# Performance work log

Hardware: AMD Instinct MI355X
Metric: run time of the kernel (lower is better)

The kernel has to match this reference:

```python
import jax, jax.numpy as jnp
import numpy as np

DIM, N_HEADS, N_EXPERTS, TOP_K = 1024, 16, 8, 2
D_FF = 4 * DIM
HEAD_DIM = DIM // N_HEADS
EPS = 1e-5


def layer_norm(x, g, b):
    m = x.mean(-1, keepdims=True)
    v = ((x - m) ** 2).mean(-1, keepdims=True)
    return (x - m) / jnp.sqrt(v + EPS) * g + b


def setup_inputs() -> dict:
    key = jax.random.key(0)
    ks = jax.random.split(key, 16)
    B, T = 8, 1024
    s = 0.02
    inp = {
        'x': jax.random.normal(ks[0], (B, T, DIM), jnp.float32),
        'attention_mask': jnp.ones((B, T), jnp.int32),
        'Wq': jax.random.normal(ks[1], (DIM, DIM), jnp.float32) * s,
        'bq': jnp.zeros((DIM,), jnp.float32),
        'Wk': jax.random.normal(ks[2], (DIM, DIM), jnp.float32) * s,
        'bk': jnp.zeros((DIM,), jnp.float32),
        'Wv': jax.random.normal(ks[3], (DIM, DIM), jnp.float32) * s,
        'bv': jnp.zeros((DIM,), jnp.float32),
        'Wo': jax.random.normal(ks[4], (DIM, DIM), jnp.float32) * s,
        'bo': jnp.zeros((DIM,), jnp.float32),
        'g1': jnp.ones((DIM,), jnp.float32),
        'beta1': jnp.zeros((DIM,), jnp.float32),
        'router_w': jax.random.normal(ks[5], (DIM, N_EXPERTS), jnp.float32) * s,
        'router_b': jnp.zeros((N_EXPERTS,), jnp.float32),
        'W1': jax.random.normal(ks[6], (N_EXPERTS, DIM, D_FF), jnp.float32) * s,
        'B1': jnp.zeros((N_EXPERTS, D_FF), jnp.float32),
        'W2': jax.random.normal(ks[7], (N_EXPERTS, D_FF, DIM), jnp.float32) * s,
        'B2': jnp.zeros((N_EXPERTS, DIM), jnp.float32),
        'g2': jnp.ones((DIM,), jnp.float32),
        'beta2': jnp.zeros((DIM,), jnp.float32),
    }
    return inp


def reference(x, attention_mask, Wq, bq, Wk, bk, Wv, bv, Wo, bo, g1, beta1,
              router_w, router_b, W1, B1, W2, B2, g2, beta2):
    B, T, D = x.shape
    H, hd = N_HEADS, HEAD_DIM
    # ---- multi-head attention with causal + padding mask ----
    q = (x @ Wq + bq).reshape(B, T, H, hd).transpose(0, 2, 1, 3)  # [B,H,T,hd]
    k = (x @ Wk + bk).reshape(B, T, H, hd).transpose(0, 2, 1, 3)
    v = (x @ Wv + bv).reshape(B, T, H, hd).transpose(0, 2, 1, 3)
    scores = jnp.einsum('bhqd,bhkd->bhqk', q, k) / jnp.sqrt(jnp.float32(hd))
    causal = jnp.tril(jnp.ones((T, T), bool))[None, None]            # [1,1,T,T]
    mask = causal & (attention_mask[:, None, None, :] != 0)         # [B,1,T,T]
    scores = jnp.where(mask, scores, jnp.float32(-1e9))
    attn = jax.nn.softmax(scores, axis=-1)
    h = jnp.einsum('bhqk,bhkd->bhqd', attn, v).transpose(0, 2, 1, 3).reshape(B, T, D)
    h = h @ Wo + bo
    # dropout is identity in eval mode
    x1 = layer_norm(x + h, g1, beta1)
    # ---- sparse top-k MoE FFN ----
    xf = x1.reshape(-1, D)                                           # [N,D]
    logits = xf @ router_w + router_b                                # [N,E]
    probs = jax.nn.softmax(logits, axis=-1)
    topv, topi = jax.lax.top_k(probs, TOP_K)                         # [N,k]
    gk = topv / topv.sum(-1, keepdims=True)                          # renormalized gates
    onehot = jax.nn.one_hot(topi, N_EXPERTS, dtype=xf.dtype)         # [N,k,E]
    gates = (onehot * gk[..., None]).sum(1)                          # [N,E]
    y = jnp.zeros_like(xf)
    for e in range(N_EXPERTS):  # fixed small expert loop
        he = jax.nn.relu(xf @ W1[e] + B1[e])
        y = y + gates[:, e:e + 1] * (he @ W2[e] + B2[e])
    # load-balancing loss: E * sum_i f_i * P_i
    f = onehot.sum(1).mean(0)                                        # fraction routed per expert
    P = probs.mean(0)
    lb = jnp.float32(N_EXPERTS) * (f * P).sum()
    out = layer_norm(x1 + y.reshape(B, T, D), g2, beta2)
    return out, lb
```

## Files before the change

### kernel.cpp

```cpp
#include <hip/hip_runtime.h>
#include <hip/hip_bf16.h>
#include <stdint.h>

#define DIMQ   1024
#define NHEADS 16
#define HD     64
#define NEXP   8
#define DFF    4096
#define NTOK   8192
#define TSEQ   1024
#define BATCH  8

typedef unsigned short u16;
typedef unsigned int   u32;
typedef __attribute__((ext_vector_type(8))) short bf16x8;
typedef __attribute__((ext_vector_type(4))) float f32x4;

__device__ __forceinline__ float bf_lo(u32 w) { return __uint_as_float(w << 16); }
__device__ __forceinline__ float bf_hi(u32 w) { return __uint_as_float(w & 0xffff0000u); }
__device__ __forceinline__ u16 f2bf(float f) {
  u32 x = __float_as_uint(f);
  return (u16)((x + 0x7fffu + ((x >> 16) & 1u)) >> 16);
}

__device__ __forceinline__ void gload16(const u16* g, u16* l) {
  __builtin_amdgcn_global_load_lds((const __attribute__((address_space(1))) u32*)g,
                                   (__attribute__((address_space(3))) u32*)l, 16, 0, 0);
}

__global__ __launch_bounds__(256) void cvt_f32_bf16(const float* __restrict__ in,
                                                    u16* __restrict__ out, int n) {
  int i = (blockIdx.x * 256 + threadIdx.x) * 4;
  if (i >= n) return;
  float4 v = *(const float4*)(in + i);
  ushort4 o;
  o.x = f2bf(v.x); o.y = f2bf(v.y); o.z = f2bf(v.z); o.w = f2bf(v.w);
  *(ushort4*)(out + i) = o;
}

__global__ __launch_bounds__(256) void transpose_f32_bf16(
    const float* __restrict__ in, u16* __restrict__ out, int R, int C) {
  __shared__ float tile[32][33];
  size_t base = (size_t)blockIdx.z * (size_t)R * (size_t)C;
  int tx = threadIdx.x & 31, ty = threadIdx.x >> 5;
  int c = blockIdx.x * 32 + tx;
#pragma unroll
  for (int i = 0; i < 4; i++) {
    int r = blockIdx.y * 32 + ty + i * 8;
    tile[ty + i * 8][tx] = in[base + (size_t)r * C + c];
  }
  __syncthreads();
  int rr = blockIdx.y * 32 + tx;
#pragma unroll
  for (int i = 0; i < 4; i++) {
    int cc = blockIdx.x * 32 + ty + i * 8;
    out[base + (size_t)cc * R + rr] = f2bf(tile[tx][ty + i * 8]);
  }
}

template <bool GATHER, bool RELU, bool TRANSC>
__device__ __forceinline__ void gemm_core(
    const u16* __restrict__ A, const u16* __restrict__ Bt,
    const float* __restrict__ bias, u16* __restrict__ C,
    int M, int N, int K, const int* __restrict__ gidx) {
  __shared__ u16 As[2][128 * 32];
  __shared__ u16 Bs[2][128 * 32];
  const int tid = threadIdx.x;
  const int lane = tid & 63;
  const int wave = tid >> 6;
  const int wr = wave >> 1, wc = wave & 1;
  const int lr = lane & 15, kg = lane >> 4;
  const int rowbase = blockIdx.y * 128;
  const int colbase = blockIdx.x * 128;

  f32x4 acc[4][4];
#pragma unroll
  for (int m = 0; m < 4; m++)
#pragma unroll
    for (int n = 0; n < 4; n++) acc[m][n] = (f32x4){0.f, 0.f, 0.f, 0.f};

  const int r0 = tid >> 2, seg = tid & 3;
  const int slog = seg ^ ((r0 >> 1) & 3);
  int ar0 = rowbase + r0;      if (ar0 >= M) ar0 = M - 1;
  int ar1 = rowbase + r0 + 64; if (ar1 >= M) ar1 = M - 1;
  const long arow0 = GATHER ? gidx[ar0] : ar0;
  const long arow1 = GATHER ? gidx[ar1] : ar1;
  const u16* Aptr0 = A + (size_t)arow0 * K + slog * 8;
  const u16* Aptr1 = A + (size_t)arow1 * K + slog * 8;
  const u16* Bptr0 = Bt + (size_t)(colbase + r0) * K + slog * 8;
  const u16* Bptr1 = Bt + (size_t)(colbase + r0 + 64) * K + slog * 8;

  const int swz = (lr >> 1) & 3;

#define STAGE128(buf, k0)                                   \
  {                                                         \
    gload16(Aptr0 + (k0), &As[buf][tid * 8]);               \
    gload16(Aptr1 + (k0), &As[buf][2048 + tid * 8]);        \
    gload16(Bptr0 + (k0), &Bs[buf][tid * 8]);               \
    gload16(Bptr1 + (k0), &Bs[buf][2048 + tid * 8]);        \
  }

  const int NT = K >> 5;
  STAGE128(0, 0);
  STAGE128(1, 32);
  for (int t = 0; t < NT; t++) {
    const int buf = t & 1;
    if (t + 1 < NT) asm volatile("s_waitcnt vmcnt(4)" ::: "memory");
    else            asm volatile("s_waitcnt vmcnt(0)" ::: "memory");
    __builtin_amdgcn_s_barrier();
    bf16x8 af[4], bfr[4];
#pragma unroll
    for (int m = 0; m < 4; m++)
      af[m] = *(const bf16x8*)(&As[buf][(wr * 64 + m * 16 + lr) * 32 + ((kg ^ swz) * 8)]);
#pragma unroll
    for (int n = 0; n < 4; n++)
      bfr[n] = *(const bf16x8*)(&Bs[buf][(wc * 64 + n * 16 + lr) * 32 + ((kg ^ swz) * 8)]);
#pragma unroll
    for (int m = 0; m < 4; m++)
#pragma unroll
      for (int n = 0; n < 4; n++)
        acc[m][n] = __builtin_amdgcn_mfma_f32_16x16x32_bf16(af[m], bfr[n], acc[m][n], 0, 0, 0);
    __builtin_amdgcn_s_barrier();
    if (t + 2 < NT) STAGE128(buf, (t + 2) << 5);
  }
#undef STAGE128

#pragma unroll
  for (int n = 0; n < 4; n++) {
    int col = colbase + wc * 64 + n * 16 + lr;
    float bv = bias[col];
#pragma unroll
    for (int m = 0; m < 4; m++) {
      int row0 = rowbase + wr * 64 + m * 16 + kg * 4;
      if (TRANSC) {
        if (row0 + 3 < M) {
          ushort4 pk;
          pk.x = f2bf(acc[m][n][0] + bv);
          pk.y = f2bf(acc[m][n][1] + bv);
          pk.z = f2bf(acc[m][n][2] + bv);
          pk.w = f2bf(acc[m][n][3] + bv);
          *(ushort4*)(&C[(size_t)col * M + row0]) = pk;
        } else {
#pragma unroll
          for (int r = 0; r < 4; r++)
            if (row0 + r < M) C[(size_t)col * M + row0 + r] = f2bf(acc[m][n][r] + bv);
        }
      } else {
#pragma unroll
        for (int r = 0; r < 4; r++) {
          int row = row0 + r;
          if (row < M) {
            float v = acc[m][n][r] + bv;
            if (RELU) v = fmaxf(v, 0.f);
            C[(size_t)row * N + col] = f2bf(v);
          }
        }
      }
    }
  }
}

__global__ __launch_bounds__(256) void gemm_bt_kernel(
    const u16* __restrict__ A, const u16* __restrict__ Bt,
    const float* __restrict__ bias, u16* __restrict__ C, int M, int N, int K) {
  gemm_core<false, false, false>(A, Bt, bias, C, M, N, K, nullptr);
}

__global__ __launch_bounds__(256) void gemm_bt_tc_kernel(
    const u16* __restrict__ A, const u16* __restrict__ Bt,
    const float* __restrict__ bias, u16* __restrict__ C, int M, int N, int K) {
  gemm_core<false, false, true>(A, Bt, bias, C, M, N, K, nullptr);
}

template <bool GATHER, bool RELU>
__device__ __forceinline__ void gemm256_core(
    const u16* __restrict__ A, const u16* __restrict__ Bt,
    const float* __restrict__ bias, u16* __restrict__ C,
    int M, int N, int K, const int* __restrict__ gidx) {
  __shared__ u16 lds[2][2][256 * 64];
  const int tid = threadIdx.x;
  const int lane = tid & 63;
  const int wave = tid >> 6;
  const int wr = wave >> 2;
  const int wcol = wave & 3;
  const int lr = lane & 15, kg = lane >> 4;
  const int rowbase = blockIdx.y * 256;
  const int colbase = blockIdx.x * 256;

  f32x4 acc[8][4];
#pragma unroll
  for (int m = 0; m < 8; m++)
#pragma unroll
    for (int n = 0; n < 4; n++) acc[m][n] = (f32x4){0.f, 0.f, 0.f, 0.f};

  const int srow0 = tid >> 3, sphys = tid & 7;
  const u16* asrc[4];
  const u16* bsrc[4];
#pragma unroll
  for (int j = 0; j < 4; j++) {
    int row = srow0 + j * 64;
    int ls = sphys ^ (row & 7);
    int ar = rowbase + row; if (ar >= M) ar = M - 1;
    long ga = GATHER ? gidx[ar] : ar;
    asrc[j] = A + (size_t)ga * K + ls * 8;
    bsrc[j] = Bt + (size_t)(colbase + row) * K + ls * 8;
  }

#define STAGE256(buf, k0)                                              \
  {                                                                    \
    _Pragma("unroll")                                                  \
    for (int j = 0; j < 4; j++) {                                      \
      gload16(asrc[j] + (k0), &lds[buf][0][tid * 8 + j * 4096]);       \
      gload16(bsrc[j] + (k0), &lds[buf][1][tid * 8 + j * 4096]);       \
    }                                                                  \
  }

  const int NT = K >> 6;
  STAGE256(0, 0);
  STAGE256(1, 64);
  for (int t = 0; t < NT; t++) {
    const int buf = t & 1;
    if (t + 1 < NT) asm volatile("s_waitcnt vmcnt(8)" ::: "memory");
    else            asm volatile("s_waitcnt vmcnt(0)" ::: "memory");
    __builtin_amdgcn_s_barrier();
    bf16x8 bfr[4][2];
#pragma unroll
    for (int nr = 0; nr < 4; nr++) {
      int rb = wcol * 64 + nr * 16 + lr;
#pragma unroll
      for (int kk = 0; kk < 2; kk++)
        bfr[nr][kk] = *(const bf16x8*)(&lds[buf][1][rb * 64 + (((kk * 4 + kg) ^ (rb & 7)) * 8)]);
    }
    __builtin_amdgcn_s_setprio(1);
#pragma unroll
    for (int mr = 0; mr < 8; mr++) {
      int ra = wr * 128 + mr * 16 + lr;
      bf16x8 a0 = *(const bf16x8*)(&lds[buf][0][ra * 64 + ((kg ^ (ra & 7)) * 8)]);
      bf16x8 a1 = *(const bf16x8*)(&lds[buf][0][ra * 64 + (((4 + kg) ^ (ra & 7)) * 8)]);
#pragma unroll
      for (int nr = 0; nr < 4; nr++) {
        acc[mr][nr] = __builtin_amdgcn_mfma_f32_16x16x32_bf16(a0, bfr[nr][0], acc[mr][nr], 0, 0, 0);
        acc[mr][nr] = __builtin_amdgcn_mfma_f32_16x16x32_bf16(a1, bfr[nr][1], acc[mr][nr], 0, 0, 0);
      }
    }
    __builtin_amdgcn_s_setprio(0);
    __builtin_amdgcn_s_barrier();
    if (t + 2 < NT) STAGE256(buf, (t + 2) << 6);
  }
#undef STAGE256

#pragma unroll
  for (int nr = 0; nr < 4; nr++) {
    int col = colbase + wcol * 64 + nr * 16 + lr;
    float bv = bias[col];
#pragma unroll
    for (int mr = 0; mr < 8; mr++) {
      int row0 = rowbase + wr * 128 + mr * 16 + kg * 4;
#pragma unroll
      for (int r = 0; r < 4; r++) {
        int row = row0 + r;
        if (row < M) {
          float v = acc[mr][nr][r] + bv;
          if (RELU) v = fmaxf(v, 0.f);
          C[(size_t)row * N + col] = f2bf(v);
        }
      }
    }
  }
}

__global__ __launch_bounds__(512, 2) void moe_gemm1_kernel(
    const u16* __restrict__ x1b, const u16* __restrict__ W1t,
    const float* __restrict__ B1, u16* __restrict__ he,
    const int* __restrict__ cnt, const int* __restrict__ off,
    const int* __restrict__ idxlist) {
  int e = blockIdx.z;
  int M = cnt[e];
  if ((int)blockIdx.y * 256 >= M) return;
  gemm256_core<true, true>(x1b, W1t + (size_t)e * DFF * DIMQ, B1 + e * DFF,
                           he + (size_t)off[e] * DFF, M, DFF, DIMQ, idxlist + off[e]);
}

__global__ __launch_bounds__(512, 2) void moe_gemm2_kernel(
    const u16* __restrict__ he, const u16* __restrict__ W2t,
    const float* __restrict__ B2, u16* __restrict__ yslot,
    const int* __restrict__ cnt, const int* __restrict__ off) {
  int e = blockIdx.z;
  int M = cnt[e];
  if ((int)blockIdx.y * 256 >= M) return;
  gemm256_core<false, false>(he + (size_t)off[e] * DFF, W2t + (size_t)e * DIMQ * DFF,
                             B2 + e * DIMQ, yslot + (size_t)off[e] * DIMQ, M, DIMQ, DFF, nullptr);
}

__global__ __launch_bounds__(256) void attn_mfma_kernel(
    const u16* __restrict__ qb, const u16* __restrict__ kb,
    const u16* __restrict__ vbT, const int* __restrict__ amask,
    u16* __restrict__ hb) {
  __shared__ u16 Ks[32 * 64];
  __shared__ u16 VTs[64 * 32];
  __shared__ u16 Ps[4][16 * 32];
  __shared__ float mbias[32];

  const int b = blockIdx.y >> 4;
  const int h = blockIdx.y & 15;
  const int qb0 = blockIdx.x * 64;
  const int tid = threadIdx.x;
  const int lane = tid & 63;
  const int wq = tid >> 6;
  const int r16 = lane & 15;
  const int kg = lane >> 4;
  const int qrow0 = qb0 + wq * 16;

  bf16x8 qf[2];
  {
    const u16* qp = qb + ((size_t)(b * TSEQ + qrow0 + r16)) * DIMQ + h * HD + kg * 8;
    qf[0] = *(const bf16x8*)(qp);
    qf[1] = *(const bf16x8*)(qp + 32);
  }
  f32x4 acc[4];
#pragma unroll
  for (int db = 0; db < 4; db++) acc[db] = (f32x4){0.f, 0.f, 0.f, 0.f};
  float m_run[4], l_run[4];
#pragma unroll
  for (int i = 0; i < 4; i++) { m_run[i] = -3.0e38f; l_run[i] = 0.f; }

  const int skey = tid >> 3, sslot = tid & 7;
  const int sd = tid >> 2, sko = tid & 3;
  const u16* kgb = kb + (size_t)(b * TSEQ) * DIMQ + h * HD;
  const u16* vgb = vbT + (size_t)(h * HD) * NTOK + (size_t)b * TSEQ;

  const int nt = (qb0 + 64) >> 5;
  for (int kt = 0; kt < nt; kt++) {
    const int k0g = kt * 32;
    __syncthreads();
    {
      uint4 kv = *(const uint4*)(kgb + (size_t)(k0g + skey) * DIMQ + sslot * 8);
      *(uint4*)(&Ks[skey * 64 + ((sslot ^ (skey & 7)) * 8)]) = kv;
      uint4 vv = *(const uint4*)(vgb + (size_t)sd * NTOK + k0g + sko * 8);
      *(uint4*)(&VTs[sd * 32 + ((sko ^ (sd & 3)) * 8)]) = vv;
      if (tid < 32) mbias[tid] = amask[b * TSEQ + k0g + tid] ? 0.f : -1e9f;
    }
    __syncthreads();
    if (k0g < qrow0 + 16) {
      f32x4 s0 = (f32x4){0.f, 0.f, 0.f, 0.f};
      f32x4 s1 = (f32x4){0.f, 0.f, 0.f, 0.f};
      {
        int key0 = r16;
        bf16x8 ka = *(const bf16x8*)(&Ks[key0 * 64 + ((kg ^ (key0 & 7)) * 8)]);
        bf16x8 kb2 = *(const bf16x8*)(&Ks[key0 * 64 + (((4 + kg) ^ (key0 & 7)) * 8)]);
        s0 = __builtin_amdgcn_mfma_f32_16x16x32_bf16(qf[0], ka, s0, 0, 0, 0);
        s0 = __builtin_amdgcn_mfma_f32_16x16x32_bf16(qf[1], kb2, s0, 0, 0, 0);
        int key1 = 16 + r16;
        bf16x8 kc = *(const bf16x8*)(&Ks[key1 * 64 + ((kg ^ (key1 & 7)) * 8)]);
        bf16x8 kd = *(const bf16x8*)(&Ks[key1 * 64 + (((4 + kg) ^ (key1 & 7)) * 8)]);
        s1 = __builtin_amdgcn_mfma_f32_16x16x32_bf16(qf[0], kc, s1, 0, 0, 0);
        s1 = __builtin_amdgcn_mfma_f32_16x16x32_bf16(qf[1], kd, s1, 0, 0, 0);
      }
      float sv0[4], sv1[4], tm[4];
      float mb0 = mbias[r16], mb1 = mbias[16 + r16];
#pragma unroll
      for (int i = 0; i < 4; i++) {
        int qg = qrow0 + kg * 4 + i;
        float a = s0[i] * 0.125f + mb0;
        float c = s1[i] * 0.125f + mb1;
        if (k0g + r16 > qg)      a = -3.0e38f;
        if (k0g + 16 + r16 > qg) c = -3.0e38f;
        sv0[i] = a; sv1[i] = c;
        tm[i] = fmaxf(a, c);
      }
#pragma unroll
      for (int mk = 1; mk < 16; mk <<= 1) {
#pragma unroll
        for (int i = 0; i < 4; i++) tm[i] = fmaxf(tm[i], __shfl_xor(tm[i], mk));
      }
      float pr0[4], pr1[4];
#pragma unroll
      for (int i = 0; i < 4; i++) {
        float nm = fmaxf(m_run[i], tm[i]);
        float sc = __expf(m_run[i] - nm);
        m_run[i] = nm;
        pr0[i] = __expf(sv0[i] - nm);
        pr1[i] = __expf(sv1[i] - nm);
        l_run[i] = l_run[i] * sc + pr0[i] + pr1[i];
#pragma unroll
        for (int db = 0; db < 4; db++) acc[db][i] *= sc;
      }
#pragma unroll
      for (int i = 0; i < 4; i++) {
        int qrl = kg * 4 + i;
        int sw = qrl & 3;
        Ps[wq][qrl * 32 + (((r16 >> 3) ^ sw) * 8) + (r16 & 7)] = f2bf(pr0[i]);
        Ps[wq][qrl * 32 + ((((16 + r16) >> 3) ^ sw) * 8) + (r16 & 7)] = f2bf(pr1[i]);
      }
      bf16x8 pf = *(const bf16x8*)(&Ps[wq][r16 * 32 + ((kg ^ (r16 & 3)) * 8)]);
#pragma unroll
      for (int db = 0; db < 4; db++) {
        int d = db * 16 + r16;
        bf16x8 vf = *(const bf16x8*)(&VTs[d * 32 + ((kg ^ (d & 3)) * 8)]);
        acc[db] = __builtin_amdgcn_mfma_f32_16x16x32_bf16(pf, vf, acc[db], 0, 0, 0);
      }
    }
  }
#pragma unroll
  for (int mk = 1; mk < 16; mk <<= 1) {
#pragma unroll
    for (int i = 0; i < 4; i++) l_run[i] += __shfl_xor(l_run[i], mk);
  }
#pragma unroll
  for (int i = 0; i < 4; i++) {
    float inv = 1.f / l_run[i];
    int qg = qrow0 + kg * 4 + i;
    u16* op = hb + ((size_t)(b * TSEQ + qg)) * DIMQ + h * HD + r16;
#pragma unroll
    for (int db = 0; db < 4; db++) op[db * 16] = f2bf(acc[db][i] * inv);
  }
}

__global__ __launch_bounds__(256) void addln_kernel(
    const float* __restrict__ xin, const u16* __restrict__ hres,
    const float* __restrict__ g, const float* __restrict__ beta,
    float* __restrict__ x1, u16* __restrict__ x1b) {
  __shared__ float red[8];
  int t = blockIdx.x;
  int d = threadIdx.x * 4;
  size_t base = (size_t)t * DIMQ + d;
  float4 xv = *(const float4*)(xin + base);
  uint2 hu = *(const uint2*)(hres + base);
  float v0 = xv.x + bf_lo(hu.x), v1 = xv.y + bf_hi(hu.x);
  float v2 = xv.z + bf_lo(hu.y), v3 = xv.w + bf_hi(hu.y);
  float s1 = v0 + v1 + v2 + v3;
  float s2 = v0 * v0 + v1 * v1 + v2 * v2 + v3 * v3;
#pragma unroll
  for (int off = 32; off; off >>= 1) {
    s1 += __shfl_down(s1, off);
    s2 += __shfl_down(s2, off);
  }
  int w = threadIdx.x >> 6;
  if ((threadIdx.x & 63) == 0) { red[w] = s1; red[4 + w] = s2; }
  __syncthreads();
  float S1 = red[0] + red[1] + red[2] + red[3];
  float S2 = red[4] + red[5] + red[6] + red[7];
  float m = S1 * (1.f / DIMQ);
  float var = S2 * (1.f / DIMQ) - m * m;
  float rs = rsqrtf(var + 1e-5f);
  float4 gv = *(const float4*)(g + d);
  float4 bv = *(const float4*)(beta + d);
  float o0 = (v0 - m) * rs * gv.x + bv.x;
  float o1 = (v1 - m) * rs * gv.y + bv.y;
  float o2 = (v2 - m) * rs * gv.z + bv.z;
  float o3 = (v3 - m) * rs * gv.w + bv.w;
  *(float4*)(x1 + base) = make_float4(o0, o1, o2, o3);
  uint2 pu;
  pu.x = (u32)f2bf(o0) | ((u32)f2bf(o1) << 16);
  pu.y = (u32)f2bf(o2) | ((u32)f2bf(o3) << 16);
  *(uint2*)(x1b + base) = pu;
}

__global__ __launch_bounds__(256) void router_kernel(
    const float* __restrict__ x1, const float* __restrict__ rw,
    const float* __restrict__ rb, int* __restrict__ topi,
    float* __restrict__ gkout, float* __restrict__ probs) {
  int t = blockIdx.x * 4 + (threadIdx.x >> 6);
  int l = threadIdx.x & 63;
  float acc[8];
#pragma unroll
  for (int e = 0; e < 8; e++) acc[e] = 0.f;
  const float* xr = x1 + (size_t)t * DIMQ;
  for (int k = l; k < DIMQ; k += 64) {
    float xv = xr[k];
    const float* w = rw + (size_t)k * 8;
#pragma unroll
    for (int e = 0; e < 8; e++) acc[e] += xv * w[e];
  }
#pragma unroll
  for (int e = 0; e < 8; e++) {
#pragma unroll
    for (int off = 32; off; off >>= 1) acc[e] += __shfl_down(acc[e], off);
  }
  if (l == 0) {
    float lg[8], p[8];
    float mx = -3e38f;
#pragma unroll
    for (int e = 0; e < 8; e++) { lg[e] = acc[e] + rb[e]; mx = fmaxf(mx, lg[e]); }
    float sum = 0.f;
#pragma unroll
    for (int e = 0; e < 8; e++) { p[e] = expf(lg[e] - mx); sum += p[e]; }
    float isum = 1.f / sum;
#pragma unroll
    for (int e = 0; e < 8; e++) p[e] *= isum;
    int e0 = 0;
#pragma unroll
    for (int e = 1; e < 8; e++) if (p[e] > p[e0]) e0 = e;
    int e1 = (e0 == 0) ? 1 : 0;
#pragma unroll
    for (int e = 0; e < 8; e++) if (e != e0 && p[e] > p[e1]) e1 = e;
    float s2 = p[e0] + p[e1];
    topi[2 * t] = e0; topi[2 * t + 1] = e1;
    gkout[2 * t] = p[e0] / s2; gkout[2 * t + 1] = p[e1] / s2;
    float* pp = probs + (size_t)t * 8;
#pragma unroll
    for (int e = 0; e < 8; e++) pp[e] = p[e];
  }
}

__global__ __launch_bounds__(256) void stats_kernel(
    const float* __restrict__ probs, const int* __restrict__ topi,
    int* __restrict__ cnt, float* __restrict__ Psum) {
  __shared__ float sps[4][8];
  __shared__ int   slc[4][8];
  float ps[8];
  int lc[8];
#pragma unroll
  for (int e = 0; e < 8; e++) { ps[e] = 0.f; lc[e] = 0; }
  int t = blockIdx.x * 256 + threadIdx.x;
  {
    const float* p = probs + (size_t)t * 8;
#pragma unroll
    for (int e = 0; e < 8; e++) ps[e] += p[e];
    lc[topi[2 * t]]++;
    lc[topi[2 * t + 1]]++;
  }
#pragma unroll
  for (int e = 0; e < 8; e++) {
#pragma unroll
    for (int off = 32; off; off >>= 1) {
      ps[e] += __shfl_down(ps[e], off);
      lc[e] += __shfl_down(lc[e], off);
    }
  }
  int w = threadIdx.x >> 6;
  if ((threadIdx.x & 63) == 0) {
#pragma unroll
    for (int e = 0; e < 8; e++) { sps[w][e] = ps[e]; slc[w][e] = lc[e]; }
  }
  __syncthreads();
  if (threadIdx.x < 8) {
    float fp = sps[0][threadIdx.x] + sps[1][threadIdx.x] + sps[2][threadIdx.x] + sps[3][threadIdx.x];
    int   fc = slc[0][threadIdx.x] + slc[1][threadIdx.x] + slc[2][threadIdx.x] + slc[3][threadIdx.x];
    atomicAdd(&Psum[threadIdx.x], fp);
    atomicAdd(&cnt[threadIdx.x], fc);
  }
}

__global__ void offsets_kernel(const int* __restrict__ cnt, const float* __restrict__ Psum,
                               int* __restrict__ off, int* __restrict__ fill,
                               float* __restrict__ lb_out) {
  if (threadIdx.x == 0 && blockIdx.x == 0) {
    int o = 0;
    float lb = 0.f;
    for (int e = 0; e < NEXP; e++) {
      off[e] = o;
      fill[e] = o;
      o += cnt[e];
      lb += ((float)cnt[e] / (float)NTOK) * (Psum[e] / (float)NTOK);
    }
    lb_out[0] = (float)NEXP * lb;
  }
}

__global__ __launch_bounds__(256) void listbuild_kernel(
    const int* __restrict__ topi, int* fill, int* __restrict__ idxlist,
    int* __restrict__ posmap) {
  __shared__ int bcnt[8];
  __shared__ int base[8];
  __shared__ int bofs[8];
  int t = blockIdx.x * 256 + threadIdx.x;
  if (threadIdx.x < 8) { bcnt[threadIdx.x] = 0; bofs[threadIdx.x] = 0; }
  __syncthreads();
  int e0 = topi[2 * t], e1 = topi[2 * t + 1];
  atomicAdd(&bcnt[e0], 1);
  atomicAdd(&bcnt[e1], 1);
  __syncthreads();
  if (threadIdx.x < 8) base[threadIdx.x] = atomicAdd(&fill[threadIdx.x], bcnt[threadIdx.x]);
  __syncthreads();
  int s0 = base[e0] + atomicAdd(&bofs[e0], 1);
  idxlist[s0] = t;
  posmap[2 * t] = s0;
  int s1 = base[e1] + atomicAdd(&bofs[e1], 1);
  idxlist[s1] = t;
  posmap[2 * t + 1] = s1;
}

__global__ __launch_bounds__(256) void finalln_kernel(
    const float* __restrict__ x1, const u16* __restrict__ yslot,
    const int* __restrict__ posmap, const float* __restrict__ gkv,
    const float* __restrict__ g, const float* __restrict__ beta,
    float* __restrict__ out) {
  __shared__ float red[8];
  int t = blockIdx.x;
  int p0 = posmap[2 * t], p1 = posmap[2 * t + 1];
  float g0 = gkv[2 * t], g1 = gkv[2 * t + 1];
  int d = threadIdx.x * 4;
  size_t base = (size_t)t * DIMQ + d;
  float4 xv = *(const float4*)(x1 + base);
  uint2 y0 = *(const uint2*)(yslot + (size_t)p0 * DIMQ + d);
  uint2 y1 = *(const uint2*)(yslot + (size_t)p1 * DIMQ + d);
  float v0 = xv.x + g0 * bf_lo(y0.x) + g1 * bf_lo(y1.x);
  float v1 = xv.y + g0 * bf_hi(y0.x) + g1 * bf_hi(y1.x);
  float v2 = xv.z + g0 * bf_lo(y0.y) + g1 * bf_lo(y1.y);
  float v3 = xv.w + g0 * bf_hi(y0.y) + g1 * bf_hi(y1.y);
  float s1 = v0 + v1 + v2 + v3;
  float s2 = v0 * v0 + v1 * v1 + v2 * v2 + v3 * v3;
#pragma unroll
  for (int off = 32; off; off >>= 1) {
    s1 += __shfl_down(s1, off);
    s2 += __shfl_down(s2, off);
  }
  int w = threadIdx.x >> 6;
  if ((threadIdx.x & 63) == 0) { red[w] = s1; red[4 + w] = s2; }
  __syncthreads();
  float S1 = red[0] + red[1] + red[2] + red[3];
  float S2 = red[4] + red[5] + red[6] + red[7];
  float m = S1 * (1.f / DIMQ);
  float var = S2 * (1.f / DIMQ) - m * m;
  float rs = rsqrtf(var + 1e-5f);
  float4 gv = *(const float4*)(g + d);
  float4 bv = *(const float4*)(beta + d);
  float4 o;
  o.x = (v0 - m) * rs * gv.x + bv.x;
  o.y = (v1 - m) * rs * gv.y + bv.y;
  o.z = (v2 - m) * rs * gv.z + bv.z;
  o.w = (v3 - m) * rs * gv.w + bv.w;
  *(float4*)(out + base) = o;
}

extern "C" void kernel_launch(void* const* d_in, const int* in_sizes, int n_in,
                              void* d_out, int out_size, void* d_ws, size_t ws_size,
                              hipStream_t stream) {
  const float* x     = (const float*)d_in[0];
  const int*   amask = (const int*)d_in[1];
  const float* Wq    = (const float*)d_in[2];
  const float* bq    = (const float*)d_in[3];
  const float* Wk    = (const float*)d_in[4];
  const float* bk    = (const float*)d_in[5];
  const float* Wv    = (const float*)d_in[6];
  const float* bv    = (const float*)d_in[7];
  const float* Wo    = (const float*)d_in[8];
  const float* bo    = (const float*)d_in[9];
  const float* g1    = (const float*)d_in[10];
  const float* beta1 = (const float*)d_in[11];
  const float* rw    = (const float*)d_in[12];
  const float* rb    = (const float*)d_in[13];
  const float* W1    = (const float*)d_in[14];
  const float* B1    = (const float*)d_in[15];
  const float* W2    = (const float*)d_in[16];
  const float* B2    = (const float*)d_in[17];
  const float* g2    = (const float*)d_in[18];
  const float* beta2 = (const float*)d_in[19];
  float* out    = (float*)d_out;
  float* lb_out = out + (size_t)NTOK * DIMQ;

  char* ws = (char*)d_ws;
  size_t off_acc = 0;
  auto alloc = [&](size_t bytes) {
    void* p = ws + off_acc;
    off_acc += (bytes + 255) & ~(size_t)255;
    return p;
  };
  u16* xb    = (u16*)alloc((size_t)NTOK * DIMQ * 2);
  u16* qbuf  = (u16*)alloc((size_t)NTOK * DIMQ * 2);
  u16* kbuf  = (u16*)alloc((size_t)NTOK * DIMQ * 2);
  u16* vbufT = (u16*)alloc((size_t)NTOK * DIMQ * 2);
  u16* hb    = (u16*)alloc((size_t)NTOK * DIMQ * 2);
  u16* ho    = (u16*)alloc((size_t)NTOK * DIMQ * 2);
  float* x1  = (float*)alloc((size_t)NTOK * DIMQ * 4);
  u16* x1b   = (u16*)alloc((size_t)NTOK * DIMQ * 2);
  u16* Wqt   = (u16*)alloc((size_t)DIMQ * DIMQ * 2);
  u16* Wkt   = (u16*)alloc((size_t)DIMQ * DIMQ * 2);
  u16* Wvt   = (u16*)alloc((size_t)DIMQ * DIMQ * 2);
  u16* Wot   = (u16*)alloc((size_t)DIMQ * DIMQ * 2);
  u16* W1t   = (u16*)alloc((size_t)NEXP * DFF * DIMQ * 2);
  u16* W2t   = (u16*)alloc((size_t)NEXP * DIMQ * DFF * 2);
  u16* he    = (u16*)alloc((size_t)2 * NTOK * DFF * 2);
  u16* yslot = (u16*)alloc((size_t)2 * NTOK * DIMQ * 2);
  char* stats = (char*)alloc(4096);
  int*   cnt   = (int*)stats;
  float* Psum  = (float*)(stats + 32);
  int*   offp  = (int*)(stats + 64);
  int*   fill  = (int*)(stats + 96);
  int* topi    = (int*)alloc((size_t)NTOK * 2 * 4);
  float* gkbuf = (float*)alloc((size_t)NTOK * 2 * 4);
  int* posmap  = (int*)alloc((size_t)NTOK * 2 * 4);
  int* idxlist = (int*)alloc((size_t)NTOK * 2 * 4);
  float* probs = (float*)alloc((size_t)NTOK * 8 * 4);

  hipMemsetAsync(stats, 0, 64, stream);

  cvt_f32_bf16<<<NTOK * DIMQ / 1024, 256, 0, stream>>>(x, xb, NTOK * DIMQ);
  transpose_f32_bf16<<<dim3(DIMQ / 32, DIMQ / 32, 1), 256, 0, stream>>>(Wq, Wqt, DIMQ, DIMQ);
  transpose_f32_bf16<<<dim3(DIMQ / 32, DIMQ / 32, 1), 256, 0, stream>>>(Wk, Wkt, DIMQ, DIMQ);
  transpose_f32_bf16<<<dim3(DIMQ / 32, DIMQ / 32, 1), 256, 0, stream>>>(Wv, Wvt, DIMQ, DIMQ);
  transpose_f32_bf16<<<dim3(DIMQ / 32, DIMQ / 32, 1), 256, 0, stream>>>(Wo, Wot, DIMQ, DIMQ);
  transpose_f32_bf16<<<dim3(DFF / 32, DIMQ / 32, NEXP), 256, 0, stream>>>(W1, W1t, DIMQ, DFF);
  transpose_f32_bf16<<<dim3(DIMQ / 32, DFF / 32, NEXP), 256, 0, stream>>>(W2, W2t, DFF, DIMQ);

  dim3 gproj(DIMQ / 128, NTOK / 128);
  gemm_bt_kernel<<<gproj, 256, 0, stream>>>(xb, Wqt, bq, qbuf, NTOK, DIMQ, DIMQ);
  gemm_bt_kernel<<<gproj, 256, 0, stream>>>(xb, Wkt, bk, kbuf, NTOK, DIMQ, DIMQ);
  gemm_bt_tc_kernel<<<gproj, 256, 0, stream>>>(xb, Wvt, bv, vbufT, NTOK, DIMQ, DIMQ);
  attn_mfma_kernel<<<dim3(TSEQ / 64, BATCH * NHEADS), 256, 0, stream>>>(qbuf, kbuf, vbufT, amask, hb);
  gemm_bt_kernel<<<gproj, 256, 0, stream>>>(hb, Wot, bo, ho, NTOK, DIMQ, DIMQ);
  addln_kernel<<<NTOK, 256, 0, stream>>>(x, ho, g1, beta1, x1, x1b);

  router_kernel<<<NTOK / 4, 256, 0, stream>>>(x1, rw, rb, topi, gkbuf, probs);
  stats_kernel<<<NTOK / 256, 256, 0, stream>>>(probs, topi, cnt, Psum);
  offsets_kernel<<<1, 64, 0, stream>>>(cnt, Psum, offp, fill, lb_out);
  listbuild_kernel<<<NTOK / 256, 256, 0, stream>>>(topi, fill, idxlist, posmap);
  moe_gemm1_kernel<<<dim3(DFF / 256, 32, NEXP), 512, 0, stream>>>(x1b, W1t, B1, he, cnt, offp, idxlist);
  moe_gemm2_kernel<<<dim3(DIMQ / 256, 32, NEXP), 512, 0, stream>>>(he, W2t, B2, yslot, cnt, offp);
  finalln_kernel<<<NTOK, 256, 0, stream>>>(x1, yslot, posmap, gkbuf, g2, beta2, out);
}
```

Before: 928.8 us.

## Use triple-buffered LDS GEMM pipelines and 64-key attention tiles

Both GEMM cores move from double to triple LDS buffering, with a single barrier per step and the next prefetch issued before the compute. The 256 GEMM's K step drops from 64 to 32, and its explicit vmcnt waits and s_setprio hints are removed. Attention now processes 64 keys per tile instead of 32, halving the tile-loop iterations and barriers at the cost of more LDS and registers. The new GEMM code relies on __syncthreads draining outstanding loads instead of fine-grained waitcnt, so some memory overlap may be lost.

```diff
diff --git a/kernel.cpp b/kernel.cpp
--- a/kernel.cpp
+++ b/kernel.cpp
@@ -63,8 +63,8 @@
     const u16* __restrict__ A, const u16* __restrict__ Bt,
     const float* __restrict__ bias, u16* __restrict__ C,
     int M, int N, int K, const int* __restrict__ gidx) {
-  __shared__ u16 As[2][128 * 32];
-  __shared__ u16 Bs[2][128 * 32];
+  __shared__ u16 As[3][128 * 32];
+  __shared__ u16 Bs[3][128 * 32];
   const int tid = threadIdx.x;
   const int lane = tid & 63;
   const int wave = tid >> 6;
@@ -103,25 +103,24 @@
   const int NT = K >> 5;
   STAGE128(0, 0);
   STAGE128(1, 32);
+  int cur = 0, stg = 2;
   for (int t = 0; t < NT; t++) {
-    const int buf = t & 1;
-    if (t + 1 < NT) asm volatile("s_waitcnt vmcnt(4)" ::: "memory");
-    else            asm volatile("s_waitcnt vmcnt(0)" ::: "memory");
-    __builtin_amdgcn_s_barrier();
+    __syncthreads();
+    if (t + 2 < NT) STAGE128(stg, (t + 2) << 5);
     bf16x8 af[4], bfr[4];
 #pragma unroll
     for (int m = 0; m < 4; m++)
-      af[m] = *(const bf16x8*)(&As[buf][(wr * 64 + m * 16 + lr) * 32 + ((kg ^ swz) * 8)]);
+      af[m] = *(const bf16x8*)(&As[cur][(wr * 64 + m * 16 + lr) * 32 + ((kg ^ swz) * 8)]);
 #pragma unroll
     for (int n = 0; n < 4; n++)
-      bfr[n] = *(const bf16x8*)(&Bs[buf][(wc * 64 + n * 16 + lr) * 32 + ((kg ^ swz) * 8)]);
+      bfr[n] = *(const bf16x8*)(&Bs[cur][(wc * 64 + n * 16 + lr) * 32 + ((kg ^ swz) * 8)]);
 #pragma unroll
     for (int m = 0; m < 4; m++)
 #pragma unroll
       for (int n = 0; n < 4; n++)
         acc[m][n] = __builtin_amdgcn_mfma_f32_16x16x32_bf16(af[m], bfr[n], acc[m][n], 0, 0, 0);
-    __builtin_amdgcn_s_barrier();
-    if (t + 2 < NT) STAGE128(buf, (t + 2) << 5);
+    cur = (cur == 2) ? 0 : cur + 1;
+    stg = (stg == 2) ? 0 : stg + 1;
   }
 #undef STAGE128
 
@@ -177,7 +176,8 @@
     const u16* __restrict__ A, const u16* __restrict__ Bt,
     const float* __restrict__ bias, u16* __restrict__ C,
     int M, int N, int K, const int* __restrict__ gidx) {
-  __shared__ u16 lds[2][2][256 * 64];
+  __shared__ u16 As[3][256 * 32];
+  __shared__ u16 Bs[3][256 * 32];
   const int tid = threadIdx.x;
   const int lane = tid & 63;
   const int wave = tid >> 6;
@@ -193,59 +193,50 @@
 #pragma unroll
     for (int n = 0; n < 4; n++) acc[m][n] = (f32x4){0.f, 0.f, 0.f, 0.f};
 
-  const int srow0 = tid >> 3, sphys = tid & 7;
-  const u16* asrc[4];
-  const u16* bsrc[4];
-#pragma unroll
-  for (int j = 0; j < 4; j++) {
-    int row = srow0 + j * 64;
-    int ls = sphys ^ (row & 7);
+  const u16* asrc[2];
+  const u16* bsrc[2];
+#pragma unroll
+  for (int j = 0; j < 2; j++) {
+    int p = tid + j * 512;
+    int row = p >> 2, sphys = p & 3;
+    int ls = sphys ^ ((row >> 1) & 3);
     int ar = rowbase + row; if (ar >= M) ar = M - 1;
     long ga = GATHER ? gidx[ar] : ar;
     asrc[j] = A + (size_t)ga * K + ls * 8;
     bsrc[j] = Bt + (size_t)(colbase + row) * K + ls * 8;
   }
 
-#define STAGE256(buf, k0)                                              \
-  {                                                                    \
-    _Pragma("unroll")                                                  \
-    for (int j = 0; j < 4; j++) {                                      \
-      gload16(asrc[j] + (k0), &lds[buf][0][tid * 8 + j * 4096]);       \
-      gload16(bsrc[j] + (k0), &lds[buf][1][tid * 8 + j * 4096]);       \
-    }                                                                  \
-  }
-
-  const int NT = K >> 6;
+#define STAGE256(buf, k0)                                      \
+  {                                                            \
+    gload16(asrc[0] + (k0), &As[buf][tid * 8]);                \
+    gload16(asrc[1] + (k0), &As[buf][4096 + tid * 8]);         \
+    gload16(bsrc[0] + (k0), &Bs[buf][tid * 8]);                \
+    gload16(bsrc[1] + (k0), &Bs[buf][4096 + tid * 8]);         \
+  }
+
+  const int NT = K >> 5;
   STAGE256(0, 0);
-  STAGE256(1, 64);
+  STAGE256(1, 32);
+  int cur = 0, stg = 2;
   for (int t = 0; t < NT; t++) {
-    const int buf = t & 1;
-    if (t + 1 < NT) asm volatile("s_waitcnt vmcnt(8)" ::: "memory");
-    else            asm volatile("s_waitcnt vmcnt(0)" ::: "memory");
-    __builtin_amdgcn_s_barrier();
-    bf16x8 bfr[4][2];
+    __syncthreads();
+    if (t + 2 < NT) STAGE256(stg, (t + 2) << 5);
+    bf16x8 bfr[4];
 #pragma unroll
     for (int nr = 0; nr < 4; nr++) {
       int rb = wcol * 64 + nr * 16 + lr;
-#pragma unroll
-      for (int kk = 0; kk < 2; kk++)
-        bfr[nr][kk] = *(const bf16x8*)(&lds[buf][1][rb * 64 + (((kk * 4 + kg) ^ (rb & 7)) * 8)]);
+      bfr[nr] = *(const bf16x8*)(&Bs[cur][rb * 32 + ((kg ^ ((rb >> 1) & 3)) * 8)]);
     }
-    __builtin_amdgcn_s_setprio(1);
 #pragma unroll
     for (int mr = 0; mr < 8; mr++) {
       int ra = wr * 128 + mr * 16 + lr;
-      bf16x8 a0 = *(const bf16x8*)(&lds[buf][0][ra * 64 + ((kg ^ (ra & 7)) * 8)]);
-      bf16x8 a1 = *(const bf16x8*)(&lds[buf][0][ra * 64 + (((4 + kg) ^ (ra & 7)) * 8)]);
-#pragma unroll
-      for (int nr = 0; nr < 4; nr++) {
-        acc[mr][nr] = __builtin_amdgcn_mfma_f32_16x16x32_bf16(a0, bfr[nr][0], acc[mr][nr], 0, 0, 0);
-        acc[mr][nr] = __builtin_amdgcn_mfma_f32_16x16x32_bf16(a1, bfr[nr][1], acc[mr][nr], 0, 0, 0);
-      }
+      bf16x8 a0 = *(const bf16x8*)(&As[cur][ra * 32 + ((kg ^ ((ra >> 1) & 3)) * 8)]);
+#pragma unroll
+      for (int nr = 0; nr < 4; nr++)
+        acc[mr][nr] = __builtin_amdgcn_mfma_f32_16x16x32_bf16(a0, bfr[nr], acc[mr][nr], 0, 0, 0);
     }
-    __builtin_amdgcn_s_setprio(0);
-    __builtin_amdgcn_s_barrier();
-    if (t + 2 < NT) STAGE256(buf, (t + 2) << 6);
+    cur = (cur == 2) ? 0 : cur + 1;
+    stg = (stg == 2) ? 0 : stg + 1;
   }
 #undef STAGE256
 
@@ -296,10 +287,10 @@
     const u16* __restrict__ qb, const u16* __restrict__ kb,
     const u16* __restrict__ vbT, const int* __restrict__ amask,
     u16* __restrict__ hb) {
-  __shared__ u16 Ks[32 * 64];
-  __shared__ u16 VTs[64 * 32];
-  __shared__ u16 Ps[4][16 * 32];
-  __shared__ float mbias[32];
+  __shared__ u16 Ks[64 * 64];
+  __shared__ u16 VTs[64 * 64];
+  __shared__ u16 Ps[4][16 * 64];
+  __shared__ float mbias[64];
 
   const int b = blockIdx.y >> 4;
   const int h = blockIdx.y & 15;
@@ -324,80 +315,85 @@
 #pragma unroll
   for (int i = 0; i < 4; i++) { m_run[i] = -3.0e38f; l_run[i] = 0.f; }
 
-  const int skey = tid >> 3, sslot = tid & 7;
-  const int sd = tid >> 2, sko = tid & 3;
+  const int kr0 = tid >> 3, ks0 = tid & 7;
+  const int kr1 = (tid + 256) >> 3, ks1 = tid & 7;
   const u16* kgb = kb + (size_t)(b * TSEQ) * DIMQ + h * HD;
   const u16* vgb = vbT + (size_t)(h * HD) * NTOK + (size_t)b * TSEQ;
 
-  const int nt = (qb0 + 64) >> 5;
+  const int nt = (qb0 + 64) >> 6;
   for (int kt = 0; kt < nt; kt++) {
-    const int k0g = kt * 32;
+    const int k0g = kt * 64;
     __syncthreads();
     {
-      uint4 kv = *(const uint4*)(kgb + (size_t)(k0g + skey) * DIMQ + sslot * 8);
-      *(uint4*)(&Ks[skey * 64 + ((sslot ^ (skey & 7)) * 8)]) = kv;
-      uint4 vv = *(const uint4*)(vgb + (size_t)sd * NTOK + k0g + sko * 8);
-      *(uint4*)(&VTs[sd * 32 + ((sko ^ (sd & 3)) * 8)]) = vv;
-      if (tid < 32) mbias[tid] = amask[b * TSEQ + k0g + tid] ? 0.f : -1e9f;
+      uint4 kv0 = *(const uint4*)(kgb + (size_t)(k0g + kr0) * DIMQ + ks0 * 8);
+      *(uint4*)(&Ks[kr0 * 64 + ((ks0 ^ (kr0 & 7)) * 8)]) = kv0;
+      uint4 kv1 = *(const uint4*)(kgb + (size_t)(k0g + kr1) * DIMQ + ks1 * 8);
+      *(uint4*)(&Ks[kr1 * 64 + ((ks1 ^ (kr1 & 7)) * 8)]) = kv1;
+      uint4 vv0 = *(const uint4*)(vgb + (size_t)kr0 * NTOK + k0g + ks0 * 8);
+      *(uint4*)(&VTs[kr0 * 64 + ((ks0 ^ (kr0 & 7)) * 8)]) = vv0;
+      uint4 vv1 = *(const uint4*)(vgb + (size_t)kr1 * NTOK + k0g + ks1 * 8);
+      *(uint4*)(&VTs[kr1 * 64 + ((ks1 ^ (kr1 & 7)) * 8)]) = vv1;
+      if (tid < 64) mbias[tid] = amask[b * TSEQ + k0g + tid] ? 0.f : -1e9f;
     }
     __syncthreads();
     if (k0g < qrow0 + 16) {
-      f32x4 s0 = (f32x4){0.f, 0.f, 0.f, 0.f};
-      f32x4 s1 = (f32x4){0.f, 0.f, 0.f, 0.f};
-      {
-        int key0 = r16;
-        bf16x8 ka = *(const bf16x8*)(&Ks[key0 * 64 + ((kg ^ (key0 & 7)) * 8)]);
-        bf16x8 kb2 = *(const bf16x8*)(&Ks[key0 * 64 + (((4 + kg) ^ (key0 & 7)) * 8)]);
-        s0 = __builtin_amdgcn_mfma_f32_16x16x32_bf16(qf[0], ka, s0, 0, 0, 0);
-        s0 = __builtin_amdgcn_mfma_f32_16x16x32_bf16(qf[1], kb2, s0, 0, 0, 0);
-        int key1 = 16 + r16;
-        bf16x8 kc = *(const bf16x8*)(&Ks[key1 * 64 + ((kg ^ (key1 & 7)) * 8)]);
-        bf16x8 kd = *(const bf16x8*)(&Ks[key1 * 64 + (((4 + kg) ^ (key1 & 7)) * 8)]);
-        s1 = __builtin_amdgcn_mfma_f32_16x16x32_bf16(qf[0], kc, s1, 0, 0, 0);
-        s1 = __builtin_amdgcn_mfma_f32_16x16x32_bf16(qf[1], kd, s1, 0, 0, 0);
+      f32x4 s[4];
+#pragma unroll
+      for (int g = 0; g < 4; g++) s[g] = (f32x4){0.f, 0.f, 0.f, 0.f};
+#pragma unroll
+      for (int g = 0; g < 4; g++) {
+        int key = g * 16 + r16;
+        bf16x8 ka  = *(const bf16x8*)(&Ks[key * 64 + ((kg ^ (key & 7)) * 8)]);
+        bf16x8 kb2 = *(const bf16x8*)(&Ks[key * 64 + (((4 + kg) ^ (key & 7)) * 8)]);
+        s[g] = __builtin_amdgcn_mfma_f32_16x16x32_bf16(qf[0], ka, s[g], 0, 0, 0);
+        s[g] = __builtin_amdgcn_mfma_f32_16x16x32_bf16(qf[1], kb2, s[g], 0, 0, 0);
       }
-      float sv0[4], sv1[4], tm[4];
-      float mb0 = mbias[r16], mb1 = mbias[16 + r16];
+      float mb[4] = {mbias[r16], mbias[16 + r16], mbias[32 + r16], mbias[48 + r16]};
+      float sv[4][4], tm[4];
 #pragma unroll
       for (int i = 0; i < 4; i++) {
         int qg = qrow0 + kg * 4 + i;
-        float a = s0[i] * 0.125f + mb0;
-        float c = s1[i] * 0.125f + mb1;
-        if (k0g + r16 > qg)      a = -3.0e38f;
-        if (k0g + 16 + r16 > qg) c = -3.0e38f;
-        sv0[i] = a; sv1[i] = c;
-        tm[i] = fmaxf(a, c);
+        tm[i] = -3.0e38f;
+#pragma unroll
+        for (int g = 0; g < 4; g++) {
+          float a = s[g][i] * 0.125f + mb[g];
+          if (k0g + g * 16 + r16 > qg) a = -3.0e38f;
+          sv[g][i] = a;
+          tm[i] = fmaxf(tm[i], a);
+        }
       }
 #pragma unroll
       for (int mk = 1; mk < 16; mk <<= 1) {
 #pragma unroll
         for (int i = 0; i < 4; i++) tm[i] = fmaxf(tm[i], __shfl_xor(tm[i], mk));
       }
-      float pr0[4], pr1[4];
 #pragma unroll
       for (int i = 0; i < 4; i++) {
         float nm = fmaxf(m_run[i], tm[i]);
         float sc = __expf(m_run[i] - nm);
         m_run[i] = nm;
-        pr0[i] = __expf(sv0[i] - nm);
-        pr1[i] = __expf(sv1[i] - nm);
-        l_run[i] = l_run[i] * sc + pr0[i] + pr1[i];
+        int qrl = kg * 4 + i;
+        float lsum = 0.f;
+#pragma unroll
+        for (int g = 0; g < 4; g++) {
+          float p = __expf(sv[g][i] - nm);
+          lsum += p;
+          int slotL = g * 2 + (r16 >> 3);
+          Ps[wq][qrl * 64 + ((slotL ^ (qrl & 7)) * 8) + (r16 & 7)] = f2bf(p);
+        }
+        l_run[i] = l_run[i] * sc + lsum;
 #pragma unroll
         for (int db = 0; db < 4; db++) acc[db][i] *= sc;
       }
-#pragma unroll
-      for (int i = 0; i < 4; i++) {
-        int qrl = kg * 4 + i;
-        int sw = qrl & 3;
-        Ps[wq][qrl * 32 + (((r16 >> 3) ^ sw) * 8) + (r16 & 7)] = f2bf(pr0[i]);
-        Ps[wq][qrl * 32 + ((((16 + r16) >> 3) ^ sw) * 8) + (r16 & 7)] = f2bf(pr1[i]);
-      }
-      bf16x8 pf = *(const bf16x8*)(&Ps[wq][r16 * 32 + ((kg ^ (r16 & 3)) * 8)]);
+      bf16x8 pf0 = *(const bf16x8*)(&Ps[wq][r16 * 64 + ((kg ^ (r16 & 7)) * 8)]);
+      bf16x8 pf1 = *(const bf16x8*)(&Ps[wq][r16 * 64 + (((4 + kg) ^ (r16 & 7)) * 8)]);
 #pragma unroll
       for (int db = 0; db < 4; db++) {
         int d = db * 16 + r16;
-        bf16x8 vf = *(const bf16x8*)(&VTs[d * 32 + ((kg ^ (d & 3)) * 8)]);
-        acc[db] = __builtin_amdgcn_mfma_f32_16x16x32_bf16(pf, vf, acc[db], 0, 0, 0);
+        bf16x8 vf0 = *(const bf16x8*)(&VTs[d * 64 + ((kg ^ (d & 7)) * 8)]);
+        bf16x8 vf1 = *(const bf16x8*)(&VTs[d * 64 + (((4 + kg) ^ (d & 7)) * 8)]);
+        acc[db] = __builtin_amdgcn_mfma_f32_16x16x32_bf16(pf0, vf0, acc[db], 0, 0, 0);
+        acc[db] = __builtin_amdgcn_mfma_f32_16x16x32_bf16(pf1, vf1, acc[db], 0, 0, 0);
       }
     }
   }
```

Measured after the change: 1.040 ms. +12.0%, slower.
